# Kernel optimization log

Hardware: AMD Instinct MI355X
Metric: run time of the kernel (lower is better)

Reference implementation:

```python
import jax, jax.numpy as jnp
import numpy as np

B, N, C = 2, 2048, 1536
H = 8
D = C // H  # 192, must match M's size


def setup_inputs() -> dict:
    key = jax.random.key(0)
    ks = jax.random.split(key, 5)
    x = jax.random.normal(ks[0], (B, N, C), dtype=jnp.float32)
    # nn.Linear(dim, 3*dim, bias=False): weight shape (3C, C)
    W_qkv = jax.random.normal(ks[1], (3 * C, C), dtype=jnp.float32) * (C ** -0.5)
    # nn.Linear(dim, dim) with bias
    W_proj = jax.random.normal(ks[2], (C, C), dtype=jnp.float32) * (C ** -0.5)
    b_proj = jnp.zeros((C,), dtype=jnp.float32)
    scale = jnp.asarray(D ** -0.5, dtype=jnp.float32)  # learned scalar, init head_dim**-0.5
    M = jnp.eye(D, dtype=jnp.float32)  # learned Mahalanobis metric, init identity
    return {"x": x, "W_qkv": W_qkv, "W_proj": W_proj, "b_proj": b_proj,
            "scale": scale, "M": M}


def reference(x, W_qkv, W_proj, b_proj, scale, M):
    Bv, Nv, Cv = x.shape
    qkv = x @ W_qkv.T                                  # [B,N,3C]
    qkv = qkv.reshape(Bv, Nv, 3, H, D).transpose(2, 0, 3, 1, 4)  # [3,B,H,N,D]
    q, k, v = qkv[0], qkv[1], qkv[2]
    q_M = q @ M                                        # [B,H,N,D]
    k_M = k @ M                                        # [B,H,N,D]
    qMq = jnp.sum(q * q_M, axis=-1, keepdims=True)     # [B,H,N,1]
    kMk = jnp.sum(k * k_M, axis=-1, keepdims=True)     # [B,H,N,1]
    kMk = jnp.swapaxes(kMk, -2, -1)                    # [B,H,1,N]
    qMk = jnp.einsum('bhnd,bhmd->bhnm', q_M, k)        # [B,H,N,N]
    dists = qMq + kMk - 2.0 * qMk                      # Mahalanobis quadratic form
    attn = jax.nn.softmax(-dists * scale, axis=-1)     # [B,H,N,N]
    out = jnp.einsum('bhnm,bhmd->bhnd', attn, v)       # [B,H,N,D]
    out = jnp.swapaxes(out, 1, 2).reshape(Bv, Nv, Cv)  # [B,N,C]
    out = out @ W_proj.T + b_proj
    return (out, attn, M)
```

## Files before the change

kernel.cpp:

```cpp
#include <hip/hip_runtime.h>

typedef _Float16 f16;
typedef __attribute__((ext_vector_type(8))) _Float16 f16x8;
typedef __attribute__((ext_vector_type(4))) float f32x4;

#define LOG2E 1.4426950408889634f
#define MFMA16(a, b, c) __builtin_amdgcn_mfma_f32_16x16x32_f16((a), (b), (c), 0, 0, 0)


__device__ __forceinline__ void gl16(const void* g, void* l) {
    __builtin_amdgcn_global_load_lds(
        (const __attribute__((address_space(1))) unsigned int*)g,
        (__attribute__((address_space(3))) unsigned int*)l, 16, 0, 0);
}

__global__ void k_cvt_all(const float* __restrict__ x, const float* __restrict__ wq,
                          const float* __restrict__ wp, f16* __restrict__ xh,
                          f16* __restrict__ wqh, f16* __restrict__ wph) {
    int i = blockIdx.x * 256 + threadIdx.x;
    const float4* s; short4* d; int off;
    if (i < 1572864) { s = (const float4*)x; d = (short4*)xh; off = i; }
    else if (i < 3342336) { s = (const float4*)wq; d = (short4*)wqh; off = i - 1572864; }
    else { s = (const float4*)wp; d = (short4*)wph; off = i - 3342336; }
    float4 v = s[off];
    union { f16 h[4]; short4 s4; } u;
    u.h[0] = (f16)v.x; u.h[1] = (f16)v.y; u.h[2] = (f16)v.z; u.h[3] = (f16)v.w;
    d[off] = u.s4;
}

__global__ void k_cvtM(const float* __restrict__ M, f16* __restrict__ Mt) {
    int i = blockIdx.x * 256 + threadIdx.x;
    if (i >= 192 * 192) return;
    int d = i / 192, e = i - (i / 192) * 192;
    Mt[d * 192 + e] = (f16)M[e * 192 + d];
}

__global__ __launch_bounds__(256) void k_gemm_qkv(
    const f16* __restrict__ A, const f16* __restrict__ Bw,
    f16* __restrict__ Qh, f16* __restrict__ Kh, f16* __restrict__ Vp)
{
    __shared__ __align__(16) char S[32768];
    const int tid = threadIdx.x, lane = tid & 63, w = tid >> 6;
    const int bid = blockIdx.x;
    const int xcd = bid & 7, cc = bid >> 3;
    const int mb = xcd * 4 + cc / 36, nb = cc - (cc / 36) * 36;
    const int m0 = mb * 128, n0 = nb * 128;
    const int sec = nb >= 24 ? 2 : (nb >= 12 ? 1 : 0);
    const int wm = (w & 1) * 64, wn = (w >> 1) * 64;
    const int L = lane & 15, g = lane >> 4;
    const char* Ab = (const char*)A;
    const char* Bb = (const char*)Bw;

    const char* gA[2]; const char* gB[2]; int ldso[2];
#pragma unroll
    for (int q = 0; q < 2; ++q) {
        int s = w * 128 + q * 64 + lane;
        int swz = ((s & 3) ^ ((s >> 2) & 3)) * 16;
        gA[q] = Ab + (size_t)(m0 + (s >> 2)) * 3072 + swz;
        gB[q] = Bb + (size_t)(n0 + (s >> 2)) * 3072 + swz;
        ldso[q] = w * 2048 + q * 1024;
    }
    const int gx = ((g ^ (L & 3)) << 4);

    f32x4 acc[4][4] = {};
#pragma unroll
    for (int q = 0; q < 2; ++q) {
        gl16(gA[q], S + ldso[q]);
        gl16(gB[q], S + 8192 + ldso[q]);
    }
    int buf = 0;
    for (int kk = 0; kk < 48; ++kk) {
        __syncthreads();
        if (kk < 47) {
            int nb_ = (buf ^ 1) * 16384;
#pragma unroll
            for (int q = 0; q < 2; ++q) {
                gl16(gA[q] + (kk + 1) * 64, S + nb_ + ldso[q]);
                gl16(gB[q] + (kk + 1) * 64, S + nb_ + 8192 + ldso[q]);
            }
        }
        const char* AsB = S + buf * 16384;
        const char* BsB = AsB + 8192;
        f16x8 af[4], bf[4];
#pragma unroll
        for (int i = 0; i < 4; ++i) {
            af[i] = *(const f16x8*)(AsB + (wm + i * 16 + L) * 64 + gx);
            bf[i] = *(const f16x8*)(BsB + (wn + i * 16 + L) * 64 + gx);
        }
        if (sec < 2) {
#pragma unroll
            for (int i = 0; i < 4; ++i)
#pragma unroll
                for (int j = 0; j < 4; ++j)
                    acc[i][j] = MFMA16(bf[j], af[i], acc[i][j]);
        } else {
#pragma unroll
            for (int i = 0; i < 4; ++i)
#pragma unroll
                for (int j = 0; j < 4; ++j)
                    acc[i][j] = MFMA16(af[i], bf[j], acc[i][j]);
        }
        buf ^= 1;
    }

    if (sec == 2) {
#pragma unroll
        for (int i = 0; i < 4; ++i)
#pragma unroll
            for (int j = 0; j < 4; ++j) {
                int rem = n0 + wn + j * 16 + L - 3072;
                int h = rem / 192, d = rem - h * 192;
                int gm = m0 + wm + i * 16 + g * 4;
                int gb = gm >> 11, nn = gm & 2047;
                union { f16 h4[4]; short4 s4; } u;
#pragma unroll
                for (int r = 0; r < 4; ++r) u.h4[r] = (f16)acc[i][j][r];
                int nnp = (nn & ~31) | (((nn >> 2) & 3) << 3) | (((nn >> 4) & 1) << 2) | (nn & 3);
                *(short4*)(Vp + (size_t)((gb * 8 + h) * 192 + d) * 2048 + nnp) = u.s4;
            }
    } else {
        f16* base = sec == 0 ? Qh : Kh;
#pragma unroll
        for (int i = 0; i < 4; ++i) {
            int gm = m0 + wm + i * 16 + L;
            int gb = gm >> 11, nn = gm & 2047;
#pragma unroll
            for (int j = 0; j < 4; ++j) {
                int rem = n0 + wn + j * 16 + g * 4 - sec * 1536;
                int h = rem / 192, d = rem - h * 192;
                union { f16 h4[4]; short4 s4; } u;
#pragma unroll
                for (int r = 0; r < 4; ++r) u.h4[r] = (f16)acc[i][j][r];
                *(short4*)(base + (size_t)((gb * 8 + h) * 2048 + nn) * 192 + d) = u.s4;
            }
        }
    }
}

__global__ __launch_bounds__(256) void k_mgemm(
    const f16* __restrict__ Qh, const f16* __restrict__ Kh,
    const f16* __restrict__ Mt, f16* __restrict__ QMh,
    const float* __restrict__ scale_p, float* __restrict__ qmq, float* __restrict__ kmk)
{
    const int tid = threadIdx.x, lane = tid & 63, w = tid >> 6;
    const int L = lane & 15, g = lane >> 4;
    const int isK = blockIdx.y;
    const f16* src = isK ? Kh : Qh;
    float* rowdot = isK ? kmk : qmq;
    const int row0 = blockIdx.x * 64 + w * 16;
    const int tokrow = row0 + L;
    f16x8 af[6];
#pragma unroll
    for (int ks = 0; ks < 6; ++ks)
        af[ks] = *(const f16x8*)((const char*)src + (size_t)tokrow * 384 + ks * 64 + g * 16);
    f32x4 acc[12] = {};
#pragma unroll
    for (int ct = 0; ct < 12; ++ct)
#pragma unroll
        for (int ks = 0; ks < 6; ++ks) {
            f16x8 bf = *(const f16x8*)((const char*)Mt + (ct * 16 + L) * 384 + ks * 64 + g * 16);
            acc[ct] = MFMA16(bf, af[ks], acc[ct]);
        }
    if (!isK) {
#pragma unroll
        for (int ct = 0; ct < 12; ++ct) {
            union { f16 h4[4]; short4 s4; } u;
#pragma unroll
            for (int r = 0; r < 4; ++r) u.h4[r] = (f16)acc[ct][r];
            *(short4*)(QMh + (size_t)tokrow * 192 + ct * 16 + g * 4) = u.s4;
        }
    }
    float s = 0.f;
#pragma unroll
    for (int ct = 0; ct < 12; ++ct) {
        union { short4 s4; f16 h[4]; } kv;
        kv.s4 = *(const short4*)(src + (size_t)tokrow * 192 + ct * 16 + g * 4);
#pragma unroll
        for (int r = 0; r < 4; ++r) s += acc[ct][r] * (float)kv.h[r];
    }
    s += __shfl_xor(s, 16); s += __shfl_xor(s, 32);
    if (lane < 16) rowdot[row0 + lane] = s * scale_p[0] * LOG2E;
}

__global__ __launch_bounds__(256) void k_attn(
    const f16* __restrict__ QMh, const f16* __restrict__ Kh,
    const f16* __restrict__ Vp, const float* __restrict__ kmk,
    const float* __restrict__ qmq, const float* __restrict__ scale_p,
    char* __restrict__ attnB, f16* __restrict__ ctx,
    float* __restrict__ lrow, float* __restrict__ mcf)
{
    __shared__ __align__(16) char KsB[2][12288];
    __shared__ __align__(16) char VsB[2][15360];
    const int tid = threadIdx.x, lane = tid & 63, w = tid >> 6;
    const int L = lane & 15, g = lane >> 4;
    const int bx = blockIdx.x;
    const int bh = (bx & 7) * 2 + (bx >> 8);
    const int qb = (bx >> 3) & 31;
    const int row0 = qb * 64 + w * 16;
    const float a2 = 2.f * scale_p[0] * LOG2E;

    const char* qbase = (const char*)QMh + (size_t)(bh * 2048 + row0) * 384;
    f16x8 qf[6];
#pragma unroll
    for (int ks = 0; ks < 6; ++ks)
        qf[ks] = *(const f16x8*)(qbase + L * 384 + ks * 64 + g * 16);
    const char* Kb = (const char*)Kh + (size_t)bh * 2048 * 384;
    const char* Vb = (const char*)Vp + (size_t)bh * 192 * 4096;
    const float* kmkrow = kmk + bh * 2048;
    const int rowi = bh * 2048 + row0 + L;
    const float Crow = qmq[rowi];

    int ksrc[3], kdst[3], vsrc[3], vdst[3];
#pragma unroll
    for (int i = 0; i < 3; ++i) {
        int s = tid + 256 * i;
        int r = s / 24, c16 = s - r * 24;
        ksrc[i] = r * 384 + c16 * 16;
        kdst[i] = r * 384 + (((c16 & ~7) | ((c16 & 7) ^ (r & 7))) << 4);
        vsrc[i] = (s >> 2) * 4096 + (s & 3) * 16;
        vdst[i] = (s >> 2) * 80 + (s & 3) * 16;
    }
    int kslot[6];
#pragma unroll
    for (int ks = 0; ks < 6; ++ks) {
        int slot = ks * 4 + g;
        kslot[ks] = (((slot & ~7) | ((slot & 7) ^ (L & 7))) << 4);
    }

    int4 stk[3], stv[3];
#pragma unroll
    for (int i = 0; i < 3; ++i) {
        stk[i] = *(const int4*)(Kb + ksrc[i]);
        stv[i] = *(const int4*)(Vb + vsrc[i]);
    }
    f32x4 cacc[12] = {};
    float lacc = 0.f;
    float m_run = -3.0e38f, scinv = 0.f;
    char* arow16 = attnB + (size_t)rowi * 8192;

    for (int c = 0; c < 64; ++c) {
        char* Kl = KsB[c & 1];
        char* Vl = VsB[c & 1];
#pragma unroll
        for (int i = 0; i < 3; ++i) {
            *(int4*)(Kl + kdst[i]) = stk[i];
            *(int4*)(Vl + vdst[i]) = stv[i];
        }
        if (c < 63) {
#pragma unroll
            for (int i = 0; i < 3; ++i) {
                stk[i] = *(const int4*)(Kb + (size_t)(c + 1) * 12288 + ksrc[i]);
                stv[i] = *(const int4*)(Vb + (size_t)(c + 1) * 64 + vsrc[i]);
            }
        }
        __syncthreads();
        f32x4 a0 = {}, a1 = {};
        __builtin_amdgcn_s_setprio(1);
#pragma unroll
        for (int ks = 0; ks < 6; ++ks) {
            f16x8 kf0 = *(const f16x8*)(Kl + L * 384 + kslot[ks]);
            f16x8 kf1 = *(const f16x8*)(Kl + (16 + L) * 384 + kslot[ks]);
            a0 = MFMA16(kf0, qf[ks], a0);
            a1 = MFMA16(kf1, qf[ks], a1);
        }
        __builtin_amdgcn_s_setprio(0);
        float4 km0 = *(const float4*)(kmkrow + c * 32 + g * 4);
        float4 km1 = *(const float4*)(kmkrow + c * 32 + 16 + g * 4);
        float e8[8];
        e8[0] = a2 * a0[0] - km0.x - Crow;
        e8[1] = a2 * a0[1] - km0.y - Crow;
        e8[2] = a2 * a0[2] - km0.z - Crow;
        e8[3] = a2 * a0[3] - km0.w - Crow;
        e8[4] = a2 * a1[0] - km1.x - Crow;
        e8[5] = a2 * a1[1] - km1.y - Crow;
        e8[6] = a2 * a1[2] - km1.z - Crow;
        e8[7] = a2 * a1[3] - km1.w - Crow;
        float mx = fmaxf(fmaxf(fmaxf(e8[0], e8[1]), fmaxf(e8[2], e8[3])),
                         fmaxf(fmaxf(e8[4], e8[5]), fmaxf(e8[6], e8[7])));
        mx = fmaxf(mx, __shfl_xor(mx, 16));
        mx = fmaxf(mx, __shfl_xor(mx, 32));
        if (__any(mx > m_run + 4.f)) {
            float mnew = fmaxf(m_run, mx);
            float fr = __builtin_amdgcn_exp2f(m_run - mnew);
            lacc *= fr;
            float frc[4];
#pragma unroll
            for (int r = 0; r < 4; ++r) frc[r] = __shfl(fr, g * 4 + r);
#pragma unroll
            for (int dt = 0; dt < 12; ++dt)
#pragma unroll
                for (int r = 0; r < 4; ++r) cacc[dt][r] *= frc[r];
            m_run = mnew;
            scinv = __builtin_amdgcn_exp2f(m_run);
        }
        if (g == 0) mcf[(size_t)c * 32768 + rowi] = scinv;
        float ps[8];
#pragma unroll
        for (int j = 0; j < 8; ++j)
            ps[j] = __builtin_amdgcn_exp2f(e8[j] - m_run);
        lacc += ((ps[0] + ps[1]) + (ps[2] + ps[3])) + ((ps[4] + ps[5]) + (ps[6] + ps[7]));
        union { f16x8 v; short4 s4[2]; } pa;
        pa.v[0] = (f16)ps[0]; pa.v[1] = (f16)ps[1]; pa.v[2] = (f16)ps[2]; pa.v[3] = (f16)ps[3];
        pa.v[4] = (f16)ps[4]; pa.v[5] = (f16)ps[5]; pa.v[6] = (f16)ps[6]; pa.v[7] = (f16)ps[7];
        *(short4*)(arow16 + c * 64 + g * 8)      = pa.s4[0];
        *(short4*)(arow16 + c * 64 + 32 + g * 8) = pa.s4[1];
        __builtin_amdgcn_s_setprio(1);
#pragma unroll
        for (int dt = 0; dt < 12; ++dt) {
            f16x8 vf = *(const f16x8*)(Vl + (dt * 16 + L) * 80 + g * 16);
            cacc[dt] = MFMA16(pa.v, vf, cacc[dt]);
        }
        __builtin_amdgcn_s_setprio(0);
    }
    lacc += __shfl_xor(lacc, 16);
    lacc += __shfl_xor(lacc, 32);
    if (g == 0) lrow[rowi] = __builtin_amdgcn_exp2f(-m_run) / lacc;
    float linv_r[4];
#pragma unroll
    for (int r = 0; r < 4; ++r) linv_r[r] = 1.f / __shfl(lacc, g * 4 + r);

    __syncthreads();
    char* scr = (char*)KsB + w * 6144;
#pragma unroll
    for (int dt = 0; dt < 12; ++dt)
#pragma unroll
        for (int r = 0; r < 4; ++r)
            *(f16*)(scr + (g * 4 + r) * 384 + (dt * 16 + L) * 2)
                = (f16)(cacc[dt][r] * linv_r[r]);
    const int b = bh >> 3, h = bh & 7;
#pragma unroll
    for (int t = 0; t < 6; ++t) {
        int chunk = t * 64 + lane;
        int tok = chunk / 24, c16 = chunk - tok * 24;
        int4 v = *(const int4*)(scr + tok * 384 + c16 * 16);
        *(int4*)((char*)ctx + ((size_t)(b * 2048 + row0 + tok) * 1536 + h * 192) * 2 + c16 * 16) = v;
    }
}

__global__ __launch_bounds__(256) void k_tail(
    const f16* __restrict__ A, const f16* __restrict__ Bw,
    const float* __restrict__ bias, float* __restrict__ out,
    char* __restrict__ attnB, const float* __restrict__ lrow,
    const float* __restrict__ mcf)
{
    const int tid = threadIdx.x;
    if (blockIdx.x >= 384) {
        const int row = (blockIdx.x - 384) * 8 + (tid >> 5);
        const int t = tid & 31;
        const float lr = lrow[row];
        char* slot = attnB + (size_t)row * 8192;
        short4 s4[16];
        float fc[16];
#pragma unroll
        for (int i = 0; i < 16; ++i) {
            s4[i] = *(const short4*)(slot + t * 8 + i * 256);
            fc[i] = mcf[(size_t)(i * 4 + (t >> 3)) * 32768 + row] * lr;
        }
        asm volatile("s_waitcnt vmcnt(0)" ::: "memory");
#pragma unroll
        for (int i = 0; i < 16; ++i) {
            union { short4 v; f16 h[4]; } u; u.v = s4[i];
            f32x4 o = { (float)u.h[0] * fc[i], (float)u.h[1] * fc[i],
                        (float)u.h[2] * fc[i], (float)u.h[3] * fc[i] };
            __builtin_nontemporal_store(o, (f32x4*)(slot + t * 16 + i * 512));
        }
        return;
    }
    __shared__ __align__(16) char S[32768];
    const int lane = tid & 63, w = tid >> 6;
    const int bid = blockIdx.x;
    const int xcd = bid & 7, cc = bid >> 3;
    const int mb = xcd * 4 + cc / 12, nbk = cc - (cc / 12) * 12;
    const int m0 = mb * 128, n0 = nbk * 128;
    const int wm = (w & 1) * 64, wn = (w >> 1) * 64;
    const int L = lane & 15, g = lane >> 4;
    const char* Ab = (const char*)A;
    const char* Bb = (const char*)Bw;

    const char* gA[2]; const char* gB[2]; int ldso[2];
#pragma unroll
    for (int q = 0; q < 2; ++q) {
        int s = w * 128 + q * 64 + lane;
        int swz = ((s & 3) ^ ((s >> 2) & 3)) * 16;
        gA[q] = Ab + (size_t)(m0 + (s >> 2)) * 3072 + swz;
        gB[q] = Bb + (size_t)(n0 + (s >> 2)) * 3072 + swz;
        ldso[q] = w * 2048 + q * 1024;
    }
    const int gx = ((g ^ (L & 3)) << 4);

    f32x4 acc[4][4] = {};
#pragma unroll
    for (int q = 0; q < 2; ++q) {
        gl16(gA[q], S + ldso[q]);
        gl16(gB[q], S + 8192 + ldso[q]);
    }
    int buf = 0;
    for (int kk = 0; kk < 48; ++kk) {
        __syncthreads();
        if (kk < 47) {
            int nb_ = (buf ^ 1) * 16384;
#pragma unroll
            for (int q = 0; q < 2; ++q) {
                gl16(gA[q] + (kk + 1) * 64, S + nb_ + ldso[q]);
                gl16(gB[q] + (kk + 1) * 64, S + nb_ + 8192 + ldso[q]);
            }
        }
        const char* AsB = S + buf * 16384;
        const char* BsB = AsB + 8192;
        f16x8 af[4], bf[4];
#pragma unroll
        for (int i = 0; i < 4; ++i) {
            af[i] = *(const f16x8*)(AsB + (wm + i * 16 + L) * 64 + gx);
            bf[i] = *(const f16x8*)(BsB + (wn + i * 16 + L) * 64 + gx);
        }
#pragma unroll
        for (int i = 0; i < 4; ++i)
#pragma unroll
            for (int j = 0; j < 4; ++j)
                acc[i][j] = MFMA16(bf[j], af[i], acc[i][j]);
        buf ^= 1;
    }
#pragma unroll
    for (int i = 0; i < 4; ++i) {
        int token = m0 + wm + i * 16 + L;
#pragma unroll
        for (int j = 0; j < 4; ++j) {
            int gnb = n0 + wn + j * 16 + g * 4;
            float4 bv = *(const float4*)(bias + gnb);
            float4 v = make_float4(acc[i][j][0] + bv.x, acc[i][j][1] + bv.y,
                                   acc[i][j][2] + bv.z, acc[i][j][3] + bv.w);
            *(float4*)(out + (size_t)token * 1536 + gnb) = v;
        }
    }
}

extern "C" void kernel_launch(void* const* d_in, const int* in_sizes, int n_in,
                              void* d_out, int out_size, void* d_ws, size_t ws_size,
                              hipStream_t stream)
{
    const float* x     = (const float*)d_in[0];
    const float* Wqkv  = (const float*)d_in[1];
    const float* Wproj = (const float*)d_in[2];
    const float* bproj = (const float*)d_in[3];
    const float* scale = (const float*)d_in[4];
    const float* M     = (const float*)d_in[5];
    float* out  = (float*)d_out;
    char* attnB = (char*)(out + 6291456);

    char* p = (char*)d_ws;
    f16* x_h     = (f16*)p;  p += 12582912;
    f16* Wqkv_h  = (f16*)p;  p += 14155776;
    f16* Wproj_h = (f16*)p;  p += 4718592;
    f16* Mt_h    = (f16*)p;  p += 73728;
    f16* Qh      = (f16*)p;  p += 12582912;
    f16* Kh      = (f16*)p;  p += 12582912;
    f16* Vp      = (f16*)p;  p += 12582912;
    f16* QMh     = (f16*)p;  p += 12582912;
    float* qmq   = (float*)p; p += 131072;
    float* kmk   = (float*)p; p += 131072;
    float* lrow  = (float*)p; p += 131072;
    float* mcf   = (float*)p; p += 8388608;
    f16* ctx     = (f16*)p;  p += 12582912;

    k_cvt_all<<<15360, 256, 0, stream>>>(x, Wqkv, Wproj, x_h, Wqkv_h, Wproj_h);
    k_cvtM<<<144, 256, 0, stream>>>(M, Mt_h);
    k_gemm_qkv<<<1152, 256, 0, stream>>>(x_h, Wqkv_h, Qh, Kh, Vp);
    k_mgemm<<<dim3(512, 2), 256, 0, stream>>>(Qh, Kh, Mt_h, QMh, scale, qmq, kmk);
    k_attn<<<512, 256, 0, stream>>>(QMh, Kh, Vp, kmk, qmq, scale, attnB, ctx, lrow, mcf);
    k_tail<<<4480, 256, 0, stream>>>(ctx, Wproj_h, bproj, out, attnB, lrow, mcf);
    hipMemcpyAsync(out + 73400320, M, 36864 * 4, hipMemcpyDeviceToDevice, stream);
}
```

Measured before the change: 388.8 us.

## Split attention key chunks across warp pairs and drop the qMq row term

The attention kernel now gives each block 32 query rows instead of 64, and launches twice as many blocks. Two warp groups each handle half of every 32-key chunk with 16x16x16 MFMAs and keep their own online-softmax state, then merge the partial context and max/sum values through shared memory. The qMq term is dropped because it cancels in the softmax, which removes its computation in k_mgemm and its load in k_attn. The V layout is no longer permuted and uses a tighter LDS pitch. In exchange, the per-chunk scale buffer doubles in size, the tail kernel reads it per key half, and each block now pays for a cross-warp merge step.

After: 566.5 us. +45.7%, slower.

```diff
diff --git a/kernel.cpp b/kernel.cpp
--- a/kernel.cpp
+++ b/kernel.cpp
@@ -2,10 +2,12 @@
 
 typedef _Float16 f16;
 typedef __attribute__((ext_vector_type(8))) _Float16 f16x8;
+typedef __attribute__((ext_vector_type(4))) _Float16 f16x4;
 typedef __attribute__((ext_vector_type(4))) float f32x4;
 
 #define LOG2E 1.4426950408889634f
 #define MFMA16(a, b, c) __builtin_amdgcn_mfma_f32_16x16x32_f16((a), (b), (c), 0, 0, 0)
+#define MFMAK16(a, b, c) __builtin_amdgcn_mfma_f32_16x16x16f16((a), (b), (c), 0, 0, 0)
 
 
 __device__ __forceinline__ void gl16(const void* g, void* l) {
@@ -115,8 +117,7 @@
                 union { f16 h4[4]; short4 s4; } u;
 #pragma unroll
                 for (int r = 0; r < 4; ++r) u.h4[r] = (f16)acc[i][j][r];
-                int nnp = (nn & ~31) | (((nn >> 2) & 3) << 3) | (((nn >> 4) & 1) << 2) | (nn & 3);
-                *(short4*)(Vp + (size_t)((gb * 8 + h) * 192 + d) * 2048 + nnp) = u.s4;
+                *(short4*)(Vp + (size_t)((gb * 8 + h) * 192 + d) * 2048 + nn) = u.s4;
             }
     } else {
         f16* base = sec == 0 ? Qh : Kh;
@@ -140,13 +141,12 @@
 __global__ __launch_bounds__(256) void k_mgemm(
     const f16* __restrict__ Qh, const f16* __restrict__ Kh,
     const f16* __restrict__ Mt, f16* __restrict__ QMh,
-    const float* __restrict__ scale_p, float* __restrict__ qmq, float* __restrict__ kmk)
+    const float* __restrict__ scale_p, float* __restrict__ kmk)
 {
     const int tid = threadIdx.x, lane = tid & 63, w = tid >> 6;
     const int L = lane & 15, g = lane >> 4;
     const int isK = blockIdx.y;
     const f16* src = isK ? Kh : Qh;
-    float* rowdot = isK ? kmk : qmq;
     const int row0 = blockIdx.x * 64 + w * 16;
     const int tokrow = row0 + L;
     f16x8 af[6];
@@ -169,6 +169,7 @@
             for (int r = 0; r < 4; ++r) u.h4[r] = (f16)acc[ct][r];
             *(short4*)(QMh + (size_t)tokrow * 192 + ct * 16 + g * 4) = u.s4;
         }
+        return;
     }
     float s = 0.f;
 #pragma unroll
@@ -179,27 +180,28 @@
         for (int r = 0; r < 4; ++r) s += acc[ct][r] * (float)kv.h[r];
     }
     s += __shfl_xor(s, 16); s += __shfl_xor(s, 32);
-    if (lane < 16) rowdot[row0 + lane] = s * scale_p[0] * LOG2E;
+    if (lane < 16) kmk[row0 + lane] = s * scale_p[0] * LOG2E;
 }
 
 __global__ __launch_bounds__(256) void k_attn(
     const f16* __restrict__ QMh, const f16* __restrict__ Kh,
     const f16* __restrict__ Vp, const float* __restrict__ kmk,
-    const float* __restrict__ qmq, const float* __restrict__ scale_p,
+    const float* __restrict__ scale_p,
     char* __restrict__ attnB, f16* __restrict__ ctx,
     float* __restrict__ lrow, float* __restrict__ mcf)
 {
-    __shared__ __align__(16) char KsB[2][12288];
-    __shared__ __align__(16) char VsB[2][15360];
+    __shared__ __align__(16) char SH[52224];
     const int tid = threadIdx.x, lane = tid & 63, w = tid >> 6;
     const int L = lane & 15, g = lane >> 4;
+    const int qg = w & 1, kg = w >> 1;
     const int bx = blockIdx.x;
-    const int bh = (bx & 7) * 2 + (bx >> 8);
-    const int qb = (bx >> 3) & 31;
-    const int row0 = qb * 64 + w * 16;
+    const int bh = (bx & 7) * 2 + (bx >> 9);
+    const int qb = (bx >> 3) & 63;
+    const int rowt = qb * 32 + qg * 16;
+    const int rowi = bh * 2048 + rowt + L;
     const float a2 = 2.f * scale_p[0] * LOG2E;
 
-    const char* qbase = (const char*)QMh + (size_t)(bh * 2048 + row0) * 384;
+    const char* qbase = (const char*)QMh + (size_t)(bh * 2048 + rowt) * 384;
     f16x8 qf[6];
 #pragma unroll
     for (int ks = 0; ks < 6; ++ks)
@@ -207,8 +209,6 @@
     const char* Kb = (const char*)Kh + (size_t)bh * 2048 * 384;
     const char* Vb = (const char*)Vp + (size_t)bh * 192 * 4096;
     const float* kmkrow = kmk + bh * 2048;
-    const int rowi = bh * 2048 + row0 + L;
-    const float Crow = qmq[rowi];
 
     int ksrc[3], kdst[3], vsrc[3], vdst[3];
 #pragma unroll
@@ -218,7 +218,7 @@
         ksrc[i] = r * 384 + c16 * 16;
         kdst[i] = r * 384 + (((c16 & ~7) | ((c16 & 7) ^ (r & 7))) << 4);
         vsrc[i] = (s >> 2) * 4096 + (s & 3) * 16;
-        vdst[i] = (s >> 2) * 80 + (s & 3) * 16;
+        vdst[i] = (s >> 2) * 72 + (s & 3) * 16;
     }
     int kslot[6];
 #pragma unroll
@@ -226,6 +226,7 @@
         int slot = ks * 4 + g;
         kslot[ks] = (((slot & ~7) | ((slot & 7) ^ (L & 7))) << 4);
     }
+    const int krow = (kg * 16 + L) * 384;
 
     int4 stk[3], stv[3];
 #pragma unroll
@@ -234,17 +235,17 @@
         stv[i] = *(const int4*)(Vb + vsrc[i]);
     }
     f32x4 cacc[12] = {};
-    float lacc = 0.f;
-    float m_run = -3.0e38f, scinv = 0.f;
+    float lacc = 0.f, m_run = -3.0e38f;
     char* arow16 = attnB + (size_t)rowi * 8192;
 
     for (int c = 0; c < 64; ++c) {
-        char* Kl = KsB[c & 1];
-        char* Vl = VsB[c & 1];
+        char* Kl = SH + (c & 1) * 12288;
+        char* Vl = SH + 24576 + (c & 1) * 13824;
 #pragma unroll
         for (int i = 0; i < 3; ++i) {
             *(int4*)(Kl + kdst[i]) = stk[i];
-            *(int4*)(Vl + vdst[i]) = stv[i];
+            *(int2*)(Vl + vdst[i])     = make_int2(stv[i].x, stv[i].y);
+            *(int2*)(Vl + vdst[i] + 8) = make_int2(stv[i].z, stv[i].w);
         }
         if (c < 63) {
 #pragma unroll
@@ -254,29 +255,21 @@
             }
         }
         __syncthreads();
-        f32x4 a0 = {}, a1 = {};
+        f32x4 a0 = {};
         __builtin_amdgcn_s_setprio(1);
 #pragma unroll
         for (int ks = 0; ks < 6; ++ks) {
-            f16x8 kf0 = *(const f16x8*)(Kl + L * 384 + kslot[ks]);
-            f16x8 kf1 = *(const f16x8*)(Kl + (16 + L) * 384 + kslot[ks]);
-            a0 = MFMA16(kf0, qf[ks], a0);
-            a1 = MFMA16(kf1, qf[ks], a1);
+            f16x8 kf = *(const f16x8*)(Kl + krow + kslot[ks]);
+            a0 = MFMA16(kf, qf[ks], a0);
         }
         __builtin_amdgcn_s_setprio(0);
-        float4 km0 = *(const float4*)(kmkrow + c * 32 + g * 4);
-        float4 km1 = *(const float4*)(kmkrow + c * 32 + 16 + g * 4);
-        float e8[8];
-        e8[0] = a2 * a0[0] - km0.x - Crow;
-        e8[1] = a2 * a0[1] - km0.y - Crow;
-        e8[2] = a2 * a0[2] - km0.z - Crow;
-        e8[3] = a2 * a0[3] - km0.w - Crow;
-        e8[4] = a2 * a1[0] - km1.x - Crow;
-        e8[5] = a2 * a1[1] - km1.y - Crow;
-        e8[6] = a2 * a1[2] - km1.z - Crow;
-        e8[7] = a2 * a1[3] - km1.w - Crow;
-        float mx = fmaxf(fmaxf(fmaxf(e8[0], e8[1]), fmaxf(e8[2], e8[3])),
-                         fmaxf(fmaxf(e8[4], e8[5]), fmaxf(e8[6], e8[7])));
+        float4 km = *(const float4*)(kmkrow + c * 32 + kg * 16 + g * 4);
+        float e4[4];
+        e4[0] = a2 * a0[0] - km.x;
+        e4[1] = a2 * a0[1] - km.y;
+        e4[2] = a2 * a0[2] - km.z;
+        e4[3] = a2 * a0[3] - km.w;
+        float mx = fmaxf(fmaxf(e4[0], e4[1]), fmaxf(e4[2], e4[3]));
         mx = fmaxf(mx, __shfl_xor(mx, 16));
         mx = fmaxf(mx, __shfl_xor(mx, 32));
         if (__any(mx > m_run + 4.f)) {
@@ -291,49 +284,67 @@
 #pragma unroll
                 for (int r = 0; r < 4; ++r) cacc[dt][r] *= frc[r];
             m_run = mnew;
-            scinv = __builtin_amdgcn_exp2f(m_run);
-        }
-        if (g == 0) mcf[(size_t)c * 32768 + rowi] = scinv;
-        float ps[8];
-#pragma unroll
-        for (int j = 0; j < 8; ++j)
-            ps[j] = __builtin_amdgcn_exp2f(e8[j] - m_run);
-        lacc += ((ps[0] + ps[1]) + (ps[2] + ps[3])) + ((ps[4] + ps[5]) + (ps[6] + ps[7]));
-        union { f16x8 v; short4 s4[2]; } pa;
+        }
+        if (g == 0) mcf[(size_t)(c * 2 + kg) * 32768 + rowi] = __builtin_amdgcn_exp2f(m_run);
+        float ps[4];
+#pragma unroll
+        for (int j = 0; j < 4; ++j)
+            ps[j] = __builtin_amdgcn_exp2f(e4[j] - m_run);
+        lacc += (ps[0] + ps[1]) + (ps[2] + ps[3]);
+        union { f16x4 v; int2 i2; } pa;
         pa.v[0] = (f16)ps[0]; pa.v[1] = (f16)ps[1]; pa.v[2] = (f16)ps[2]; pa.v[3] = (f16)ps[3];
-        pa.v[4] = (f16)ps[4]; pa.v[5] = (f16)ps[5]; pa.v[6] = (f16)ps[6]; pa.v[7] = (f16)ps[7];
-        *(short4*)(arow16 + c * 64 + g * 8)      = pa.s4[0];
-        *(short4*)(arow16 + c * 64 + 32 + g * 8) = pa.s4[1];
+        *(int2*)(arow16 + c * 64 + kg * 32 + g * 8) = pa.i2;
         __builtin_amdgcn_s_setprio(1);
 #pragma unroll
         for (int dt = 0; dt < 12; ++dt) {
-            f16x8 vf = *(const f16x8*)(Vl + (dt * 16 + L) * 80 + g * 16);
-            cacc[dt] = MFMA16(pa.v, vf, cacc[dt]);
+            f16x4 vf = *(const f16x4*)(Vl + (dt * 16 + L) * 72 + kg * 32 + g * 8);
+            cacc[dt] = MFMAK16(pa.v, vf, cacc[dt]);
         }
         __builtin_amdgcn_s_setprio(0);
     }
     lacc += __shfl_xor(lacc, 16);
     lacc += __shfl_xor(lacc, 32);
-    if (g == 0) lrow[rowi] = __builtin_amdgcn_exp2f(-m_run) / lacc;
-    float linv_r[4];
-#pragma unroll
-    for (int r = 0; r < 4; ++r) linv_r[r] = 1.f / __shfl(lacc, g * 4 + r);
 
     __syncthreads();
-    char* scr = (char*)KsB + w * 6144;
-#pragma unroll
-    for (int dt = 0; dt < 12; ++dt)
-#pragma unroll
-        for (int r = 0; r < 4; ++r)
-            *(f16*)(scr + (g * 4 + r) * 384 + (dt * 16 + L) * 2)
-                = (f16)(cacc[dt][r] * linv_r[r]);
-    const int b = bh >> 3, h = bh & 7;
-#pragma unroll
-    for (int t = 0; t < 6; ++t) {
-        int chunk = t * 64 + lane;
-        int tok = chunk / 24, c16 = chunk - tok * 24;
-        int4 v = *(const int4*)(scr + tok * 384 + c16 * 16);
-        *(int4*)((char*)ctx + ((size_t)(b * 2048 + row0 + tok) * 1536 + h * 192) * 2 + c16 * 16) = v;
+    float* hdr = (float*)(SH + 24576);
+    float* cb  = (float*)SH;
+    if (kg == 1) {
+        if (g == 0) { hdr[qg * 32 + L] = m_run; hdr[qg * 32 + 16 + L] = lacc; }
+        float* my = cb + (qg * 64 + lane) * 48;
+#pragma unroll
+        for (int dt = 0; dt < 12; ++dt) *(f32x4*)(my + dt * 4) = cacc[dt];
+    }
+    __syncthreads();
+    if (kg == 0) {
+        float m1 = hdr[qg * 32 + L], l1 = hdr[qg * 32 + 16 + L];
+        float mt = fmaxf(m_run, m1);
+        float w0 = __builtin_amdgcn_exp2f(m_run - mt);
+        float w1 = __builtin_amdgcn_exp2f(m1 - mt);
+        float lt = lacc * w0 + l1 * w1;
+        if (g == 0) lrow[rowi] = __builtin_amdgcn_exp2f(-mt) / lt;
+        float f0 = w0 / lt, f1 = w1 / lt;
+        float f0r[4], f1r[4];
+#pragma unroll
+        for (int r = 0; r < 4; ++r) {
+            f0r[r] = __shfl(f0, g * 4 + r);
+            f1r[r] = __shfl(f1, g * 4 + r);
+        }
+        const float* other = cb + (qg * 64 + lane) * 48;
+        char* scr = SH + 24576 + 2048 + qg * 6144;
+#pragma unroll
+        for (int dt = 0; dt < 12; ++dt)
+#pragma unroll
+            for (int r = 0; r < 4; ++r)
+                *(f16*)(scr + (g * 4 + r) * 384 + (dt * 16 + L) * 2)
+                    = (f16)(cacc[dt][r] * f0r[r] + other[dt * 4 + r] * f1r[r]);
+        const int b = bh >> 3, h = bh & 7;
+#pragma unroll
+        for (int t = 0; t < 6; ++t) {
+            int chunk = t * 64 + lane;
+            int tok = chunk / 24, c16 = chunk - tok * 24;
+            int4 v = *(const int4*)(scr + tok * 384 + c16 * 16);
+            *(int4*)((char*)ctx + ((size_t)(b * 2048 + rowt + tok) * 1536 + h * 192) * 2 + c16 * 16) = v;
+        }
     }
 }
 
@@ -354,7 +365,8 @@
 #pragma unroll
         for (int i = 0; i < 16; ++i) {
             s4[i] = *(const short4*)(slot + t * 8 + i * 256);
-            fc[i] = mcf[(size_t)(i * 4 + (t >> 3)) * 32768 + row] * lr;
+            int chunk = i * 4 + (t >> 3), kg = (t >> 2) & 1;
+            fc[i] = mcf[(size_t)(chunk * 2 + kg) * 32768 + row] * lr;
         }
         asm volatile("s_waitcnt vmcnt(0)" ::: "memory");
 #pragma unroll
@@ -456,17 +468,16 @@
     f16* Kh      = (f16*)p;  p += 12582912;
     f16* Vp      = (f16*)p;  p += 12582912;
     f16* QMh     = (f16*)p;  p += 12582912;
-    float* qmq   = (float*)p; p += 131072;
     float* kmk   = (float*)p; p += 131072;
     float* lrow  = (float*)p; p += 131072;
-    float* mcf   = (float*)p; p += 8388608;
+    float* mcf   = (float*)p; p += 16777216;
     f16* ctx     = (f16*)p;  p += 12582912;
 
     k_cvt_all<<<15360, 256, 0, stream>>>(x, Wqkv, Wproj, x_h, Wqkv_h, Wproj_h);
     k_cvtM<<<144, 256, 0, stream>>>(M, Mt_h);
     k_gemm_qkv<<<1152, 256, 0, stream>>>(x_h, Wqkv_h, Qh, Kh, Vp);
-    k_mgemm<<<dim3(512, 2), 256, 0, stream>>>(Qh, Kh, Mt_h, QMh, scale, qmq, kmk);
-    k_attn<<<512, 256, 0, stream>>>(QMh, Kh, Vp, kmk, qmq, scale, attnB, ctx, lrow, mcf);
+    k_mgemm<<<dim3(512, 2), 256, 0, stream>>>(Qh, Kh, Mt_h, QMh, scale, kmk);
+    k_attn<<<1024, 256, 0, stream>>>(QMh, Kh, Vp, kmk, scale, attnB, ctx, lrow, mcf);
     k_tail<<<4480, 256, 0, stream>>>(ctx, Wproj_h, bproj, out, attnB, lrow, mcf);
     hipMemcpyAsync(out + 73400320, M, 36864 * 4, hipMemcpyDeviceToDevice, stream);
 }
```
